# Kernel optimization log

Measured on AMD Instinct MI355X. Metric: run time of the kernel, lower is better.

Reference implementation:

```python
import jax, jax.numpy as jnp
import numpy as np

ED = 200      # entity/relation dim
KW = 9        # kernel width
OC = 32       # out channels
WOUT = ED - KW + 1  # 192 valid-conv output width
B = 1024
NE = 40943
NR = 18


def setup_inputs() -> dict:
    key = jax.random.key(0)
    ks = jax.random.split(key, 9)
    g = lambda k, shape: jax.random.normal(k, shape, jnp.float32) * 0.05
    return dict(
        e1_idx=jax.random.randint(ks[0], (B,), 0, NE, dtype=jnp.int32),
        r_idx=jax.random.randint(ks[1], (B,), 0, NR, dtype=jnp.int32),
        W1=g(ks[2], (ED, KW * OC)),
        b1=g(ks[3], (KW * OC,)),
        W2=g(ks[4], (WOUT * OC, ED)),
        b2=g(ks[5], (ED,)),
        bias_logits=g(ks[6], (NE,)),
        E=g(ks[7], (NE, ED)),
        R=g(ks[8], (NR, ED)),
    )


def reference(e1_idx, r_idx, W1, b1, W2, b2, bias_logits, E, R):
    e1 = E[e1_idx]          # [B, 200]
    r = R[r_idx]            # [B, 200]
    # hypernetwork: relation -> per-sample conv filters [B, KW, OC]
    k = (r @ W1 + b1).reshape(-1, KW, OC)
    # per-sample valid 1D conv of e1 with its own filters (depthwise-as-groups trick collapsed)
    idx = jnp.arange(WOUT)[:, None] + jnp.arange(KW)[None, :]  # [WOUT, KW]
    patches = e1[:, idx]                                        # [B, WOUT, KW]
    # flatten order matches TF: (out_channel major, width minor)
    feat = jnp.einsum('bwj,bjo->bow', patches, k).reshape(e1.shape[0], OC * WOUT)
    h = jax.nn.relu(feat @ W2 + b2)                             # [B, 200]
    logits = h @ E.T + bias_logits                              # [B, NE]
    return logits
```

## Files before the change

kernel.cpp:

```cpp
#include <hip/hip_runtime.h>

#define NE 40943
#define NR 18
#define ED 200
#define KWC 9
#define OC 32
#define WOUT 192
#define KOC 288
#define KFEAT 6144
#define KH 224
#define G1_LD 136
#define G2_LD 40

typedef unsigned short u16;
typedef unsigned int u32;
typedef __bf16 bf16x8 __attribute__((ext_vector_type(8)));
typedef float f32x4 __attribute__((ext_vector_type(4)));
typedef u16 u16x8 __attribute__((ext_vector_type(8)));
typedef u16 u16x4 __attribute__((ext_vector_type(4)));

__device__ __forceinline__ u16 f2bf(float f) {
  u32 u = __builtin_bit_cast(u32, f);
  u32 r = (u + 0x7fffu + ((u >> 16) & 1u)) >> 16;
  return (u16)r;
}

__global__ void prep_k_kernel(const float* __restrict__ R,
                              const float* __restrict__ W1,
                              const float* __restrict__ b1,
                              float* __restrict__ Kr) {
  int rel = blockIdx.x;
  int j = threadIdx.x;
  float acc = b1[j];
  const float* rrow = R + rel * ED;
  for (int d = 0; d < ED; ++d) acc += rrow[d] * W1[d * KOC + j];
  Kr[rel * KOC + j] = acc;
}

__global__ void prep_feat_kernel(const int* __restrict__ e1_idx,
                                 const int* __restrict__ r_idx,
                                 const float* __restrict__ E,
                                 const float* __restrict__ Kr,
                                 u16* __restrict__ feat) {
  __shared__ float e1s[ED];
  __shared__ float ks[KOC];
  int b = blockIdx.y;
  int t = threadIdx.x;
  int e1 = e1_idx[b];
  int r = r_idx[b];
  if (t < ED) e1s[t] = E[(size_t)e1 * ED + t];
  ks[t] = Kr[r * KOC + t];
  if (t < KOC - 256) ks[256 + t] = Kr[r * KOC + 256 + t];
  __syncthreads();
  int i0 = (blockIdx.x * 256 + t) * 4;
  int o = i0 / WOUT;
  int w0 = i0 % WOUT;
  float a0 = 0.f, a1 = 0.f, a2 = 0.f, a3 = 0.f;
#pragma unroll
  for (int j = 0; j < KWC; ++j) {
    float kv = ks[j * OC + o];
    a0 += e1s[w0 + j] * kv;
    a1 += e1s[w0 + 1 + j] * kv;
    a2 += e1s[w0 + 2 + j] * kv;
    a3 += e1s[w0 + 3 + j] * kv;
  }
  u16x4 st = {f2bf(a0), f2bf(a1), f2bf(a2), f2bf(a3)};
  *(u16x4*)(feat + (size_t)b * KFEAT + i0) = st;
}

__global__ void conv_w2t_kernel(const float* __restrict__ W2, u16* __restrict__ W2T) {
  __shared__ float tile[32][33];
  int i0 = blockIdx.x * 32;
  int d0 = blockIdx.y * 32;
  int tx = threadIdx.x & 31;
  int ty = threadIdx.x >> 5;
#pragma unroll
  for (int rr = 0; rr < 4; ++rr) {
    int i = i0 + ty + rr * 8;
    int d = d0 + tx;
    float v = (d < ED) ? W2[(size_t)i * ED + d] : 0.f;
    tile[tx][ty + rr * 8] = v;
  }
  __syncthreads();
#pragma unroll
  for (int rr = 0; rr < 4; ++rr) {
    int d = d0 + ty + rr * 8;
    int i = i0 + tx;
    W2T[(size_t)d * KFEAT + i] = f2bf(tile[ty + rr * 8][tx]);
  }
}

__global__ void conv_e_kernel(const float* __restrict__ E, u16* __restrict__ Eb) {
  int idx = blockIdx.x * 256 + threadIdx.x;
  const int total = NE * (KH / 4);
  if (idx >= total) return;
  int row = idx / (KH / 4);
  int c4 = (idx % (KH / 4)) * 4;
  u16x4 st = {0, 0, 0, 0};
  if (c4 < ED) {
    f32x4 v = *(const f32x4*)(E + (size_t)row * ED + c4);
    st[0] = f2bf(v[0]); st[1] = f2bf(v[1]); st[2] = f2bf(v[2]); st[3] = f2bf(v[3]);
  }
  *(u16x4*)(Eb + (size_t)row * KH + c4) = st;
}

__global__ __launch_bounds__(256) void gemm1_kernel(
    const u16* __restrict__ A,
    const u16* __restrict__ B,
    const float* __restrict__ b2,
    u16* __restrict__ H) {
  __shared__ u16 lA[64 * G1_LD];
  __shared__ u16 lB[64 * G1_LD];
  const int t = threadIdx.x;
  const int m0 = blockIdx.y * 64;
  const int n0 = blockIdx.x * 64;
  const int wave = t >> 6, lane = t & 63;
  const int wm = (wave >> 1) * 32, wn = (wave & 1) * 32;
  const int lr = lane & 15, lq = lane >> 4;
  f32x4 zero = {0.f, 0.f, 0.f, 0.f};
  f32x4 acc[2][2];
#pragma unroll
  for (int i = 0; i < 2; ++i)
#pragma unroll
    for (int j = 0; j < 2; ++j) acc[i][j] = zero;

  for (int k0 = 0; k0 < KFEAT; k0 += 128) {
#pragma unroll
    for (int s = 0; s < 4; ++s) {
      int v = t + s * 256;
      int r = v >> 4;
      int c8 = (v & 15) * 8;
      *(u16x8*)(lA + r * G1_LD + c8) = *(const u16x8*)(A + (size_t)(m0 + r) * KFEAT + k0 + c8);
      *(u16x8*)(lB + r * G1_LD + c8) = *(const u16x8*)(B + (size_t)(n0 + r) * KFEAT + k0 + c8);
    }
    __syncthreads();
#pragma unroll
    for (int kk = 0; kk < 128; kk += 32) {
      bf16x8 af[2], bfv[2];
#pragma unroll
      for (int mi = 0; mi < 2; ++mi)
        af[mi] = *(const bf16x8*)(lA + (wm + mi * 16 + lr) * G1_LD + kk + lq * 8);
#pragma unroll
      for (int ni = 0; ni < 2; ++ni)
        bfv[ni] = *(const bf16x8*)(lB + (wn + ni * 16 + lr) * G1_LD + kk + lq * 8);
#pragma unroll
      for (int mi = 0; mi < 2; ++mi)
#pragma unroll
        for (int ni = 0; ni < 2; ++ni)
          acc[mi][ni] = __builtin_amdgcn_mfma_f32_16x16x32_bf16(af[mi], bfv[ni], acc[mi][ni], 0, 0, 0);
    }
    __syncthreads();
  }
#pragma unroll
  for (int mi = 0; mi < 2; ++mi) {
    int row = m0 + wm + mi * 16 + lq * 4;
#pragma unroll
    for (int ni = 0; ni < 2; ++ni) {
      int col = n0 + wn + ni * 16 + lr;
      if (col < KH) {
        float bv = (col < ED) ? b2[col] : 0.f;
#pragma unroll
        for (int i = 0; i < 4; ++i) {
          float vv = acc[mi][ni][i] + bv;
          vv = vv > 0.f ? vv : 0.f;
          if (col >= ED) vv = 0.f;
          H[(size_t)(row + i) * KH + col] = f2bf(vv);
        }
      }
    }
  }
}

__global__ __launch_bounds__(256) void gemm2_kernel(
    const u16* __restrict__ Hb,
    const u16* __restrict__ Eb,
    const float* __restrict__ bias,
    float* __restrict__ out) {
  __shared__ u16 lA[128 * G2_LD];
  __shared__ u16 lB[128 * G2_LD];
  const int t = threadIdx.x;
  const int m0 = blockIdx.y * 128;
  const int n0 = blockIdx.x * 128;
  const int wave = t >> 6, lane = t & 63;
  const int wm = (wave >> 1) * 64, wn = (wave & 1) * 64;
  const int lr = lane & 15, lq = lane >> 4;
  f32x4 zero = {0.f, 0.f, 0.f, 0.f};
  f32x4 acc[4][4];
#pragma unroll
  for (int i = 0; i < 4; ++i)
#pragma unroll
    for (int j = 0; j < 4; ++j) acc[i][j] = zero;

  for (int k0 = 0; k0 < KH; k0 += 32) {
#pragma unroll
    for (int s = 0; s < 2; ++s) {
      int v = t + s * 256;
      int r = v >> 2;
      int c8 = (v & 3) * 8;
      *(u16x8*)(lA + r * G2_LD + c8) = *(const u16x8*)(Hb + (size_t)(m0 + r) * KH + k0 + c8);
      int gr = n0 + r;
      u16x8 bv = {0, 0, 0, 0, 0, 0, 0, 0};
      if (gr < NE) bv = *(const u16x8*)(Eb + (size_t)gr * KH + k0 + c8);
      *(u16x8*)(lB + r * G2_LD + c8) = bv;
    }
    __syncthreads();
    bf16x8 af[4], bfv[4];
#pragma unroll
    for (int mi = 0; mi < 4; ++mi)
      af[mi] = *(const bf16x8*)(lA + (wm + mi * 16 + lr) * G2_LD + lq * 8);
#pragma unroll
    for (int ni = 0; ni < 4; ++ni)
      bfv[ni] = *(const bf16x8*)(lB + (wn + ni * 16 + lr) * G2_LD + lq * 8);
#pragma unroll
    for (int mi = 0; mi < 4; ++mi)
#pragma unroll
      for (int ni = 0; ni < 4; ++ni)
        acc[mi][ni] = __builtin_amdgcn_mfma_f32_16x16x32_bf16(af[mi], bfv[ni], acc[mi][ni], 0, 0, 0);
    __syncthreads();
  }
#pragma unroll
  for (int mi = 0; mi < 4; ++mi) {
    int row = m0 + wm + mi * 16 + lq * 4;
#pragma unroll
    for (int ni = 0; ni < 4; ++ni) {
      int col = n0 + wn + ni * 16 + lr;
      if (col < NE) {
        float bv = bias[col];
#pragma unroll
        for (int i = 0; i < 4; ++i)
          out[(size_t)(row + i) * NE + col] = acc[mi][ni][i] + bv;
      }
    }
  }
}

extern "C" void kernel_launch(void* const* d_in, const int* in_sizes, int n_in,
                              void* d_out, int out_size, void* d_ws, size_t ws_size,
                              hipStream_t stream) {
  const int* e1_idx = (const int*)d_in[0];
  const int* r_idx = (const int*)d_in[1];
  const float* W1 = (const float*)d_in[2];
  const float* b1 = (const float*)d_in[3];
  const float* W2 = (const float*)d_in[4];
  const float* b2 = (const float*)d_in[5];
  const float* bias_logits = (const float*)d_in[6];
  const float* E = (const float*)d_in[7];
  const float* R = (const float*)d_in[8];
  float* out = (float*)d_out;

  char* ws = (char*)d_ws;
  float* Kr = (float*)ws;
  u16* feat = (u16*)(ws + 32768);
  u16* W2T = (u16*)(ws + 32768 + 12582912);
  u16* Hb = (u16*)(ws + 32768 + 12582912 + 3145728);
  u16* Eb = (u16*)(ws + 32768 + 12582912 + 3145728 + 458752);

  prep_k_kernel<<<dim3(NR), dim3(KOC), 0, stream>>>(R, W1, b1, Kr);
  conv_w2t_kernel<<<dim3(KFEAT / 32, 256 / 32), dim3(256), 0, stream>>>(W2, W2T);
  conv_e_kernel<<<dim3((NE * (KH / 4) + 255) / 256), dim3(256), 0, stream>>>(E, Eb);
  prep_feat_kernel<<<dim3(KFEAT / 1024, 1024), dim3(256), 0, stream>>>(e1_idx, r_idx, E, Kr, feat);
  gemm1_kernel<<<dim3(4, 16), dim3(256), 0, stream>>>(feat, W2T, b2, Hb);
  gemm2_kernel<<<dim3((NE + 127) / 128, 8), dim3(256), 0, stream>>>(Hb, Eb, bias_logits, out);
}
```

Baseline: 340.9 us.

## Fold hypernetwork conv and W2 into per-relation matrices, drop GEMM1

Since there are only 18 relations, the per-sample convolution followed by the W2 projection is precomputed as a 200x200 matrix per relation. A simple per-sample kernel then computes h = relu(e1 @ C[r] + b2) in fp32. This removes the large bf16 feature buffer, the W2 transpose and the K=6144 MFMA GEMM. In exchange it adds a scalar build kernel with strided W2 reads and repeated C-slice reads per sample.

```diff
diff --git a/kernel.cpp b/kernel.cpp
--- a/kernel.cpp
+++ b/kernel.cpp
@@ -7,9 +7,7 @@
 #define OC 32
 #define WOUT 192
 #define KOC 288
-#define KFEAT 6144
 #define KH 224
-#define G1_LD 136
 #define G2_LD 40
 
 typedef unsigned short u16;
@@ -28,65 +26,64 @@
 __global__ void prep_k_kernel(const float* __restrict__ R,
                               const float* __restrict__ W1,
                               const float* __restrict__ b1,
-                              float* __restrict__ Kr) {
+                              float* __restrict__ KrT) {
   int rel = blockIdx.x;
   int j = threadIdx.x;
   float acc = b1[j];
   const float* rrow = R + rel * ED;
   for (int d = 0; d < ED; ++d) acc += rrow[d] * W1[d * KOC + j];
-  Kr[rel * KOC + j] = acc;
+  KrT[j * NR + rel] = acc;
 }
 
-__global__ void prep_feat_kernel(const int* __restrict__ e1_idx,
-                                 const int* __restrict__ r_idx,
-                                 const float* __restrict__ E,
-                                 const float* __restrict__ Kr,
-                                 u16* __restrict__ feat) {
-  __shared__ float e1s[ED];
-  __shared__ float ks[KOC];
-  int b = blockIdx.y;
-  int t = threadIdx.x;
-  int e1 = e1_idx[b];
-  int r = r_idx[b];
-  if (t < ED) e1s[t] = E[(size_t)e1 * ED + t];
-  ks[t] = Kr[r * KOC + t];
-  if (t < KOC - 256) ks[256 + t] = Kr[r * KOC + 256 + t];
-  __syncthreads();
-  int i0 = (blockIdx.x * 256 + t) * 4;
-  int o = i0 / WOUT;
-  int w0 = i0 % WOUT;
-  float a0 = 0.f, a1 = 0.f, a2 = 0.f, a3 = 0.f;
+__global__ __launch_bounds__(256) void build_c_kernel(const float* __restrict__ KrT,
+                                                      const float* __restrict__ W2,
+                                                      float* __restrict__ C) {
+  int p = blockIdx.x;
+  int d = threadIdx.x;
+  int jlo = p > (WOUT - 1) ? p - (WOUT - 1) : 0;
+  int jhi = p < (KWC - 1) ? p : (KWC - 1);
+  if (d < ED) {
+    float acc[NR];
 #pragma unroll
-  for (int j = 0; j < KWC; ++j) {
-    float kv = ks[j * OC + o];
-    a0 += e1s[w0 + j] * kv;
-    a1 += e1s[w0 + 1 + j] * kv;
-    a2 += e1s[w0 + 2 + j] * kv;
-    a3 += e1s[w0 + 3 + j] * kv;
+    for (int r = 0; r < NR; ++r) acc[r] = 0.f;
+    for (int j = jlo; j <= jhi; ++j) {
+      int w = p - j;
+      const float* w2base = W2 + (size_t)w * ED + d;
+      const float* kb = KrT + (j * OC) * NR;
+#pragma unroll
+      for (int o = 0; o < OC; ++o) {
+        float w2v = w2base[(size_t)o * WOUT * ED];
+#pragma unroll
+        for (int r = 0; r < NR; ++r) acc[r] += kb[o * NR + r] * w2v;
+      }
+    }
+#pragma unroll
+    for (int r = 0; r < NR; ++r) C[((size_t)r * ED + p) * ED + d] = acc[r];
   }
-  u16x4 st = {f2bf(a0), f2bf(a1), f2bf(a2), f2bf(a3)};
-  *(u16x4*)(feat + (size_t)b * KFEAT + i0) = st;
 }
 
-__global__ void conv_w2t_kernel(const float* __restrict__ W2, u16* __restrict__ W2T) {
-  __shared__ float tile[32][33];
-  int i0 = blockIdx.x * 32;
-  int d0 = blockIdx.y * 32;
-  int tx = threadIdx.x & 31;
-  int ty = threadIdx.x >> 5;
-#pragma unroll
-  for (int rr = 0; rr < 4; ++rr) {
-    int i = i0 + ty + rr * 8;
-    int d = d0 + tx;
-    float v = (d < ED) ? W2[(size_t)i * ED + d] : 0.f;
-    tile[tx][ty + rr * 8] = v;
-  }
+__global__ __launch_bounds__(256) void h_kernel(const int* __restrict__ e1_idx,
+                                                const int* __restrict__ r_idx,
+                                                const float* __restrict__ E,
+                                                const float* __restrict__ C,
+                                                const float* __restrict__ b2,
+                                                u16* __restrict__ Hb) {
+  __shared__ float e1s[ED];
+  int b = blockIdx.x;
+  int t = threadIdx.x;
+  if (t < ED) e1s[t] = E[(size_t)e1_idx[b] * ED + t];
   __syncthreads();
-#pragma unroll
-  for (int rr = 0; rr < 4; ++rr) {
-    int d = d0 + ty + rr * 8;
-    int i = i0 + tx;
-    W2T[(size_t)d * KFEAT + i] = f2bf(tile[ty + rr * 8][tx]);
+  int r = r_idx[b];
+  const float* Cr = C + (size_t)r * ED * ED;
+  if (t < KH) {
+    float acc = 0.f;
+    if (t < ED) {
+#pragma unroll 8
+      for (int p = 0; p < ED; ++p) acc += e1s[p] * Cr[(size_t)p * ED + t];
+      acc += b2[t];
+      acc = acc > 0.f ? acc : 0.f;
+    }
+    Hb[(size_t)b * KH + t] = (t < ED) ? f2bf(acc) : (u16)0;
   }
 }
 
@@ -102,73 +99,6 @@
     st[0] = f2bf(v[0]); st[1] = f2bf(v[1]); st[2] = f2bf(v[2]); st[3] = f2bf(v[3]);
   }
   *(u16x4*)(Eb + (size_t)row * KH + c4) = st;
-}
-
-__global__ __launch_bounds__(256) void gemm1_kernel(
-    const u16* __restrict__ A,
-    const u16* __restrict__ B,
-    const float* __restrict__ b2,
-    u16* __restrict__ H) {
-  __shared__ u16 lA[64 * G1_LD];
-  __shared__ u16 lB[64 * G1_LD];
-  const int t = threadIdx.x;
-  const int m0 = blockIdx.y * 64;
-  const int n0 = blockIdx.x * 64;
-  const int wave = t >> 6, lane = t & 63;
-  const int wm = (wave >> 1) * 32, wn = (wave & 1) * 32;
-  const int lr = lane & 15, lq = lane >> 4;
-  f32x4 zero = {0.f, 0.f, 0.f, 0.f};
-  f32x4 acc[2][2];
-#pragma unroll
-  for (int i = 0; i < 2; ++i)
-#pragma unroll
-    for (int j = 0; j < 2; ++j) acc[i][j] = zero;
-
-  for (int k0 = 0; k0 < KFEAT; k0 += 128) {
-#pragma unroll
-    for (int s = 0; s < 4; ++s) {
-      int v = t + s * 256;
-      int r = v >> 4;
-      int c8 = (v & 15) * 8;
-      *(u16x8*)(lA + r * G1_LD + c8) = *(const u16x8*)(A + (size_t)(m0 + r) * KFEAT + k0 + c8);
-      *(u16x8*)(lB + r * G1_LD + c8) = *(const u16x8*)(B + (size_t)(n0 + r) * KFEAT + k0 + c8);
-    }
-    __syncthreads();
-#pragma unroll
-    for (int kk = 0; kk < 128; kk += 32) {
-      bf16x8 af[2], bfv[2];
-#pragma unroll
-      for (int mi = 0; mi < 2; ++mi)
-        af[mi] = *(const bf16x8*)(lA + (wm + mi * 16 + lr) * G1_LD + kk + lq * 8);
-#pragma unroll
-      for (int ni = 0; ni < 2; ++ni)
-        bfv[ni] = *(const bf16x8*)(lB + (wn + ni * 16 + lr) * G1_LD + kk + lq * 8);
-#pragma unroll
-      for (int mi = 0; mi < 2; ++mi)
-#pragma unroll
-        for (int ni = 0; ni < 2; ++ni)
-          acc[mi][ni] = __builtin_amdgcn_mfma_f32_16x16x32_bf16(af[mi], bfv[ni], acc[mi][ni], 0, 0, 0);
-    }
-    __syncthreads();
-  }
-#pragma unroll
-  for (int mi = 0; mi < 2; ++mi) {
-    int row = m0 + wm + mi * 16 + lq * 4;
-#pragma unroll
-    for (int ni = 0; ni < 2; ++ni) {
-      int col = n0 + wn + ni * 16 + lr;
-      if (col < KH) {
-        float bv = (col < ED) ? b2[col] : 0.f;
-#pragma unroll
-        for (int i = 0; i < 4; ++i) {
-          float vv = acc[mi][ni][i] + bv;
-          vv = vv > 0.f ? vv : 0.f;
-          if (col >= ED) vv = 0.f;
-          H[(size_t)(row + i) * KH + col] = f2bf(vv);
-        }
-      }
-    }
-  }
 }
 
 __global__ __launch_bounds__(256) void gemm2_kernel(
@@ -249,16 +179,14 @@
   float* out = (float*)d_out;
 
   char* ws = (char*)d_ws;
-  float* Kr = (float*)ws;
-  u16* feat = (u16*)(ws + 32768);
-  u16* W2T = (u16*)(ws + 32768 + 12582912);
-  u16* Hb = (u16*)(ws + 32768 + 12582912 + 3145728);
-  u16* Eb = (u16*)(ws + 32768 + 12582912 + 3145728 + 458752);
+  float* KrT = (float*)ws;
+  float* C = (float*)(ws + 32768);
+  u16* Hb = (u16*)(ws + 32768 + 2880000);
+  u16* Eb = (u16*)(ws + 32768 + 2880000 + 458752);
 
-  prep_k_kernel<<<dim3(NR), dim3(KOC), 0, stream>>>(R, W1, b1, Kr);
-  conv_w2t_kernel<<<dim3(KFEAT / 32, 256 / 32), dim3(256), 0, stream>>>(W2, W2T);
+  prep_k_kernel<<<dim3(NR), dim3(KOC), 0, stream>>>(R, W1, b1, KrT);
+  build_c_kernel<<<dim3(ED), dim3(256), 0, stream>>>(KrT, W2, C);
+  h_kernel<<<dim3(1024), dim3(256), 0, stream>>>(e1_idx, r_idx, E, C, b2, Hb);
   conv_e_kernel<<<dim3((NE * (KH / 4) + 255) / 256), dim3(256), 0, stream>>>(E, Eb);
-  prep_feat_kernel<<<dim3(KFEAT / 1024, 1024), dim3(256), 0, stream>>>(e1_idx, r_idx, E, Kr, feat);
-  gemm1_kernel<<<dim3(4, 16), dim3(256), 0, stream>>>(feat, W2T, b2, Hb);
   gemm2_kernel<<<dim3((NE + 127) / 128, 8), dim3(256), 0, stream>>>(Hb, Eb, bias_logits, out);
 }
```

Measured after the change: 320.4 us. -6.0%, faster.
